# Performance work log

Measured on AMD Instinct MI355X. Metric: run time of the kernel, lower is better.

Reference implementation:

```python
import jax, jax.numpy as jnp
import numpy as np

B, T, D, A = 64, 2048, 512, 128

def setup_inputs() -> dict:
    key = jax.random.key(0)
    k_x, k_w1, k_b1, k_w2, k_b2 = jax.random.split(key, 5)
    s1 = 1.0 / np.sqrt(D)
    s2 = 1.0 / np.sqrt(A)
    return {
        "x": jax.random.normal(k_x, (B, T, D), dtype=jnp.float32),
        "W1": jax.random.uniform(k_w1, (D, A), minval=-s1, maxval=s1, dtype=jnp.float32),
        "b1": jax.random.uniform(k_b1, (A,), minval=-s1, maxval=s1, dtype=jnp.float32),
        "W2": jax.random.uniform(k_w2, (A, 1), minval=-s2, maxval=s2, dtype=jnp.float32),
        "b2": jax.random.uniform(k_b2, (1,), minval=-s2, maxval=s2, dtype=jnp.float32),
    }

def reference(x, W1, b1, W2, b2):
    # attention scores: [B, T, 1]
    h = jnp.tanh(jnp.einsum('btd,da->bta', x, W1) + b1)
    scores = jnp.einsum('bta,ao->bto', h, W2) + b2
    w = jax.nn.softmax(scores, axis=1)              # [B, T, 1]
    mu = jnp.sum(x * w, axis=1)                     # [B, D]
    var = jnp.sum((x - mu[:, None, :]) ** 2 * w, axis=1)
    std = jnp.sqrt(var + 1e-6)
    return jnp.concatenate([mu, std], axis=-1)      # [B, 2D]
```

## Files before the change

kernel.cpp:

```cpp
#include <hip/hip_runtime.h>
#include <hip/hip_bf16.h>
#include <math.h>

#define B_ 64
#define T_ 2048
#define D_ 512
#define A_ 128

typedef __bf16 bf16x8 __attribute__((ext_vector_type(8)));
typedef float  f32x4  __attribute__((ext_vector_type(4)));

__global__ __launch_bounds__(256) void prep_kernel(
    const float* __restrict__ W1, __hip_bfloat16* __restrict__ W1T)
{
    int idx = blockIdx.x * 256 + threadIdx.x;
    int k = idx >> 7;
    int n = idx & 127;
    W1T[n * D_ + k] = __float2bfloat16(W1[idx]);
}

__device__ inline bf16x8 cvt8(float4 a, float4 b) {
    bf16x8 r;
    r[0] = (__bf16)a.x; r[1] = (__bf16)a.y; r[2] = (__bf16)a.z; r[3] = (__bf16)a.w;
    r[4] = (__bf16)b.x; r[5] = (__bf16)b.y; r[6] = (__bf16)b.z; r[7] = (__bf16)b.w;
    return r;
}

__device__ inline float fast_tanh(float v) {
    v = fminf(fmaxf(v, -15.f), 15.f);
    float e = __expf(2.f * v);
    return (e - 1.f) / (e + 1.f);
}

__global__ __launch_bounds__(256) void scores_kernel(
    const float* __restrict__ x, const __hip_bfloat16* __restrict__ W1T_,
    const float* __restrict__ b1, const float* __restrict__ W2,
    const float* __restrict__ b2, float* __restrict__ scores)
{
    const __bf16* W1T = (const __bf16*)W1T_;
    const int tid  = threadIdx.x;
    const int wave = tid >> 6;
    const int lane = tid & 63;
    const int col  = lane & 15;
    const int kgrp = lane >> 4;

    const long tokbase = (long)blockIdx.x * 128 + wave * 32;

    f32x4 acc[8][2];
#pragma unroll
    for (int mt = 0; mt < 8; mt++) {
        acc[mt][0] = (f32x4){0.f, 0.f, 0.f, 0.f};
        acc[mt][1] = (f32x4){0.f, 0.f, 0.f, 0.f};
    }

    const float* xp0 = x + (tokbase + col) * D_;
    const float* xp1 = xp0 + 16 * D_;
    const __bf16* wp = W1T + (long)col * D_;

#pragma unroll 2
    for (int ks = 0; ks < 16; ks++) {
        const int klane = ks * 32 + kgrp * 8;
        float4 b0a = *(const float4*)(xp0 + klane);
        float4 b0b = *(const float4*)(xp0 + klane + 4);
        float4 b1a = *(const float4*)(xp1 + klane);
        float4 b1b = *(const float4*)(xp1 + klane + 4);
        bf16x8 bf0 = cvt8(b0a, b0b);
        bf16x8 bf1 = cvt8(b1a, b1b);
#pragma unroll
        for (int mt = 0; mt < 8; mt++) {
            bf16x8 af = *(const bf16x8*)(wp + (long)mt * 16 * D_ + klane);
            acc[mt][0] = __builtin_amdgcn_mfma_f32_16x16x32_bf16(af, bf0, acc[mt][0], 0, 0, 0);
            acc[mt][1] = __builtin_amdgcn_mfma_f32_16x16x32_bf16(af, bf1, acc[mt][1], 0, 0, 0);
        }
    }

    float p0 = 0.f, p1 = 0.f;
#pragma unroll
    for (int mt = 0; mt < 8; mt++) {
#pragma unroll
        for (int r = 0; r < 4; r++) {
            int n = mt * 16 + kgrp * 4 + r;
            float bb = b1[n];
            float ww = W2[n];
            p0 += fast_tanh(acc[mt][0][r] + bb) * ww;
            p1 += fast_tanh(acc[mt][1][r] + bb) * ww;
        }
    }
    p0 += __shfl_xor(p0, 16, 64);
    p0 += __shfl_xor(p0, 32, 64);
    p1 += __shfl_xor(p1, 16, 64);
    p1 += __shfl_xor(p1, 32, 64);
    if (lane < 16) {
        float bias = b2[0];
        scores[tokbase + col]      = p0 + bias;
        scores[tokbase + 16 + col] = p1 + bias;
    }
}

__global__ __launch_bounds__(256) void softmax_kernel(
    const float* __restrict__ scores, float* __restrict__ w)
{
    const int b = blockIdx.x;
    const int tid = threadIdx.x;
    const float* s = scores + (long)b * T_;

    float v[8];
    float mx = -1e30f;
#pragma unroll
    for (int j = 0; j < 8; j++) {
        v[j] = s[tid + j * 256];
        mx = fmaxf(mx, v[j]);
    }
#pragma unroll
    for (int off = 1; off < 64; off <<= 1)
        mx = fmaxf(mx, __shfl_xor(mx, off, 64));
    __shared__ float redm[4];
    if ((tid & 63) == 0) redm[tid >> 6] = mx;
    __syncthreads();
    mx = fmaxf(fmaxf(redm[0], redm[1]), fmaxf(redm[2], redm[3]));

    float sum = 0.f;
#pragma unroll
    for (int j = 0; j < 8; j++) {
        v[j] = __expf(v[j] - mx);
        sum += v[j];
    }
#pragma unroll
    for (int off = 1; off < 64; off <<= 1)
        sum += __shfl_xor(sum, off, 64);
    __shared__ float reds[4];
    if ((tid & 63) == 0) reds[tid >> 6] = sum;
    __syncthreads();
    sum = reds[0] + reds[1] + reds[2] + reds[3];
    const float inv = 1.0f / sum;
#pragma unroll
    for (int j = 0; j < 8; j++)
        w[(long)b * T_ + tid + j * 256] = v[j] * inv;
}

__global__ __launch_bounds__(256) void pool_partial_kernel(
    const float* __restrict__ x, const float* __restrict__ w,
    float* __restrict__ pmu, float* __restrict__ pm2)
{
    const int blk = blockIdx.x;
    const int b = blk >> 3;
    const int t0 = (blk & 7) * 256;
    const int tid = threadIdx.x;
    const int half = tid >> 7;
    const int dq = tid & 127;

    const float* wb = w + (long)b * T_ + t0;
    const float* xb = x + ((long)b * T_ + t0) * D_ + dq * 4;

    float4 mu = {0.f, 0.f, 0.f, 0.f};
    float4 m2 = {0.f, 0.f, 0.f, 0.f};

#pragma unroll 4
    for (int t = half; t < 256; t += 2) {
        float wt = wb[t];
        float4 xv = *(const float4*)(xb + (long)t * D_);
        mu.x = fmaf(wt, xv.x, mu.x);
        mu.y = fmaf(wt, xv.y, mu.y);
        mu.z = fmaf(wt, xv.z, mu.z);
        mu.w = fmaf(wt, xv.w, mu.w);
        m2.x = fmaf(wt * xv.x, xv.x, m2.x);
        m2.y = fmaf(wt * xv.y, xv.y, m2.y);
        m2.z = fmaf(wt * xv.z, xv.z, m2.z);
        m2.w = fmaf(wt * xv.w, xv.w, m2.w);
    }

    __shared__ float4 smu[256];
    __shared__ float4 sm2[256];
    smu[tid] = mu;
    sm2[tid] = m2;
    __syncthreads();

    if (tid < 128) {
        float4 a = smu[tid], c = smu[tid + 128];
        float4 e = sm2[tid], f = sm2[tid + 128];
        a.x += c.x; a.y += c.y; a.z += c.z; a.w += c.w;
        e.x += f.x; e.y += f.y; e.z += f.z; e.w += f.w;
        *(float4*)(pmu + (long)blk * D_ + dq * 4) = a;
        *(float4*)(pm2 + (long)blk * D_ + dq * 4) = e;
    }
}

__global__ __launch_bounds__(256) void pool_final_kernel(
    const float* __restrict__ pmu, const float* __restrict__ pm2,
    float* __restrict__ out)
{
    const int b = blockIdx.x;
    const int tid = threadIdx.x;
#pragma unroll
    for (int i = 0; i < 2; i++) {
        int d = tid + i * 256;
        float mu = 0.f, m2 = 0.f;
#pragma unroll
        for (int c = 0; c < 8; c++) {
            mu += pmu[((long)b * 8 + c) * D_ + d];
            m2 += pm2[((long)b * 8 + c) * D_ + d];
        }
        out[(long)b * (2 * D_) + d] = mu;
        out[(long)b * (2 * D_) + D_ + d] = sqrtf(fmaxf(m2 - mu * mu, 0.f) + 1e-6f);
    }
}

extern "C" void kernel_launch(void* const* d_in, const int* in_sizes, int n_in,
                              void* d_out, int out_size, void* d_ws, size_t ws_size,
                              hipStream_t stream) {
    const float* x  = (const float*)d_in[0];
    const float* W1 = (const float*)d_in[1];
    const float* b1 = (const float*)d_in[2];
    const float* W2 = (const float*)d_in[3];
    const float* b2 = (const float*)d_in[4];
    float* out = (float*)d_out;

    float* ws = (float*)d_ws;
    float* scores = ws;
    float* w      = ws + (long)B_ * T_;
    float* pmu    = ws + 2L * B_ * T_;
    float* pm2    = pmu + 512L * D_;
    __hip_bfloat16* W1T = (__hip_bfloat16*)(pm2 + 512L * D_);

    prep_kernel<<<256, 256, 0, stream>>>(W1, W1T);
    scores_kernel<<<(B_ * T_) / 128, 256, 0, stream>>>(x, W1T, b1, W2, b2, scores);
    softmax_kernel<<<B_, 256, 0, stream>>>(scores, w);
    pool_partial_kernel<<<B_ * 8, 256, 0, stream>>>(x, w, pmu, pm2);
    pool_final_kernel<<<B_, 256, 0, stream>>>(pmu, pm2, out);
}
```

Before: 428.2 us.

## Stage W1 in LDS and widen token tile per wave in scores kernel

The scores kernel now stages 128-column K chunks of the bf16 W1 transpose in padded shared memory and has each wave process 64 tokens instead of 32. Each W1 fragment then feeds four MFMAs instead of two, and the per-wave global reloads of W1 go away. The pooling partial kernel is split into 16 chunks per batch instead of 8 to raise parallelism, and the workspace offsets and final reduction are adjusted to match. The costs are more accumulator registers (a launch-bounds hint of 2 blocks per SM is added), extra barriers per K chunk, and half as many scores blocks.

```diff
diff --git a/kernel.cpp b/kernel.cpp
--- a/kernel.cpp
+++ b/kernel.cpp
@@ -18,6 +18,9 @@
     int n = idx & 127;
     W1T[n * D_ + k] = __float2bfloat16(W1[idx]);
 }
+
+#define KC 128
+#define KPAD 136
 
 __device__ inline bf16x8 cvt8(float4 a, float4 b) {
     bf16x8 r;
@@ -32,11 +35,13 @@
     return (e - 1.f) / (e + 1.f);
 }
 
-__global__ __launch_bounds__(256) void scores_kernel(
+__global__ __launch_bounds__(256, 2) void scores_kernel(
     const float* __restrict__ x, const __hip_bfloat16* __restrict__ W1T_,
     const float* __restrict__ b1, const float* __restrict__ W2,
     const float* __restrict__ b2, float* __restrict__ scores)
 {
+    __shared__ __bf16 w1s[A_][KPAD];
+
     const __bf16* W1T = (const __bf16*)W1T_;
     const int tid  = threadIdx.x;
     const int wave = tid >> 6;
@@ -44,37 +49,54 @@
     const int col  = lane & 15;
     const int kgrp = lane >> 4;
 
-    const long tokbase = (long)blockIdx.x * 128 + wave * 32;
-
-    f32x4 acc[8][2];
-#pragma unroll
-    for (int mt = 0; mt < 8; mt++) {
-        acc[mt][0] = (f32x4){0.f, 0.f, 0.f, 0.f};
-        acc[mt][1] = (f32x4){0.f, 0.f, 0.f, 0.f};
-    }
-
-    const float* xp0 = x + (tokbase + col) * D_;
-    const float* xp1 = xp0 + 16 * D_;
-    const __bf16* wp = W1T + (long)col * D_;
-
-#pragma unroll 2
-    for (int ks = 0; ks < 16; ks++) {
-        const int klane = ks * 32 + kgrp * 8;
-        float4 b0a = *(const float4*)(xp0 + klane);
-        float4 b0b = *(const float4*)(xp0 + klane + 4);
-        float4 b1a = *(const float4*)(xp1 + klane);
-        float4 b1b = *(const float4*)(xp1 + klane + 4);
-        bf16x8 bf0 = cvt8(b0a, b0b);
-        bf16x8 bf1 = cvt8(b1a, b1b);
-#pragma unroll
-        for (int mt = 0; mt < 8; mt++) {
-            bf16x8 af = *(const bf16x8*)(wp + (long)mt * 16 * D_ + klane);
-            acc[mt][0] = __builtin_amdgcn_mfma_f32_16x16x32_bf16(af, bf0, acc[mt][0], 0, 0, 0);
-            acc[mt][1] = __builtin_amdgcn_mfma_f32_16x16x32_bf16(af, bf1, acc[mt][1], 0, 0, 0);
-        }
-    }
-
-    float p0 = 0.f, p1 = 0.f;
+    const long tokbase = (long)blockIdx.x * 256 + wave * 64;
+
+    f32x4 acc[8][4];
+#pragma unroll
+    for (int mt = 0; mt < 8; mt++)
+#pragma unroll
+        for (int tt = 0; tt < 4; tt++)
+            acc[mt][tt] = (f32x4){0.f, 0.f, 0.f, 0.f};
+
+    const float* xp = x + (tokbase + col) * D_;
+
+    for (int kc = 0; kc < D_; kc += KC) {
+        __syncthreads();
+        {
+            int n = tid >> 4;
+#pragma unroll
+            for (int i = 0; i < 8; i++) {
+                int idx = tid + i * 256;
+                int row = idx >> 4;
+                int kslot = idx & 15;
+                *(bf16x8*)&w1s[row][kslot * 8] =
+                    *(const bf16x8*)(W1T + (long)row * D_ + kc + kslot * 8);
+            }
+            (void)n;
+        }
+        __syncthreads();
+
+#pragma unroll
+        for (int ks = 0; ks < 4; ks++) {
+            const int klane = kc + ks * 32 + kgrp * 8;
+            bf16x8 bf[4];
+#pragma unroll
+            for (int tt = 0; tt < 4; tt++) {
+                float4 a = *(const float4*)(xp + (long)tt * 16 * D_ + klane);
+                float4 b = *(const float4*)(xp + (long)tt * 16 * D_ + klane + 4);
+                bf[tt] = cvt8(a, b);
+            }
+#pragma unroll
+            for (int mt = 0; mt < 8; mt++) {
+                bf16x8 af = *(const bf16x8*)&w1s[mt * 16 + col][ks * 32 + kgrp * 8];
+#pragma unroll
+                for (int tt = 0; tt < 4; tt++)
+                    acc[mt][tt] = __builtin_amdgcn_mfma_f32_16x16x32_bf16(af, bf[tt], acc[mt][tt], 0, 0, 0);
+            }
+        }
+    }
+
+    float p[4] = {0.f, 0.f, 0.f, 0.f};
 #pragma unroll
     for (int mt = 0; mt < 8; mt++) {
 #pragma unroll
@@ -82,18 +104,21 @@
             int n = mt * 16 + kgrp * 4 + r;
             float bb = b1[n];
             float ww = W2[n];
-            p0 += fast_tanh(acc[mt][0][r] + bb) * ww;
-            p1 += fast_tanh(acc[mt][1][r] + bb) * ww;
-        }
-    }
-    p0 += __shfl_xor(p0, 16, 64);
-    p0 += __shfl_xor(p0, 32, 64);
-    p1 += __shfl_xor(p1, 16, 64);
-    p1 += __shfl_xor(p1, 32, 64);
+#pragma unroll
+            for (int tt = 0; tt < 4; tt++)
+                p[tt] += fast_tanh(acc[mt][tt][r] + bb) * ww;
+        }
+    }
+#pragma unroll
+    for (int tt = 0; tt < 4; tt++) {
+        p[tt] += __shfl_xor(p[tt], 16, 64);
+        p[tt] += __shfl_xor(p[tt], 32, 64);
+    }
     if (lane < 16) {
         float bias = b2[0];
-        scores[tokbase + col]      = p0 + bias;
-        scores[tokbase + 16 + col] = p1 + bias;
+#pragma unroll
+        for (int tt = 0; tt < 4; tt++)
+            scores[tokbase + tt * 16 + col] = p[tt] + bias;
     }
 }
 
@@ -143,8 +168,8 @@
     float* __restrict__ pmu, float* __restrict__ pm2)
 {
     const int blk = blockIdx.x;
-    const int b = blk >> 3;
-    const int t0 = (blk & 7) * 256;
+    const int b = blk >> 4;
+    const int t0 = (blk & 15) * 128;
     const int tid = threadIdx.x;
     const int half = tid >> 7;
     const int dq = tid & 127;
@@ -156,7 +181,7 @@
     float4 m2 = {0.f, 0.f, 0.f, 0.f};
 
 #pragma unroll 4
-    for (int t = half; t < 256; t += 2) {
+    for (int t = half; t < 128; t += 2) {
         float wt = wb[t];
         float4 xv = *(const float4*)(xb + (long)t * D_);
         mu.x = fmaf(wt, xv.x, mu.x);
@@ -196,9 +221,9 @@
         int d = tid + i * 256;
         float mu = 0.f, m2 = 0.f;
 #pragma unroll
-        for (int c = 0; c < 8; c++) {
-            mu += pmu[((long)b * 8 + c) * D_ + d];
-            m2 += pm2[((long)b * 8 + c) * D_ + d];
+        for (int c = 0; c < 16; c++) {
+            mu += pmu[((long)b * 16 + c) * D_ + d];
+            m2 += pm2[((long)b * 16 + c) * D_ + d];
         }
         out[(long)b * (2 * D_) + d] = mu;
         out[(long)b * (2 * D_) + D_ + d] = sqrtf(fmaxf(m2 - mu * mu, 0.f) + 1e-6f);
@@ -219,12 +244,12 @@
     float* scores = ws;
     float* w      = ws + (long)B_ * T_;
     float* pmu    = ws + 2L * B_ * T_;
-    float* pm2    = pmu + 512L * D_;
-    __hip_bfloat16* W1T = (__hip_bfloat16*)(pm2 + 512L * D_);
+    float* pm2    = pmu + 1024L * D_;
+    __hip_bfloat16* W1T = (__hip_bfloat16*)(pm2 + 1024L * D_);
 
     prep_kernel<<<256, 256, 0, stream>>>(W1, W1T);
-    scores_kernel<<<(B_ * T_) / 128, 256, 0, stream>>>(x, W1T, b1, W2, b2, scores);
+    scores_kernel<<<(B_ * T_) / 256, 256, 0, stream>>>(x, W1T, b1, W2, b2, scores);
     softmax_kernel<<<B_, 256, 0, stream>>>(scores, w);
-    pool_partial_kernel<<<B_ * 8, 256, 0, stream>>>(x, w, pmu, pm2);
+    pool_partial_kernel<<<B_ * 16, 256, 0, stream>>>(x, w, pmu, pm2);
     pool_final_kernel<<<B_, 256, 0, stream>>>(pmu, pm2, out);
 }
```

Result: slower. 445.1 us (+3.9%).

## Fuse scores, softmax and pooling into one chunked kernel with deferred normalization

Applied to the files above, without the earlier changes.

Merges the score GEMM, softmax and weighted pooling into one kernel per 64-token chunk. Each chunk computes unnormalized exp(score) weights and accumulates weighted partial sums, and the finalize kernel divides by the summed partition. The aim is to read x from HBM once instead of twice and to drop two kernel launches. The risk is that exp without max subtraction can overflow for large scores, and finalize now reduces 32 chunks per batch instead of 8.

```diff
diff --git a/kernel.cpp b/kernel.cpp
--- a/kernel.cpp
+++ b/kernel.cpp
@@ -6,6 +6,8 @@
 #define T_ 2048
 #define D_ 512
 #define A_ 128
+#define CHUNK 64
+#define NCHUNK (T_ / CHUNK)
 
 typedef __bf16 bf16x8 __attribute__((ext_vector_type(8)));
 typedef float  f32x4  __attribute__((ext_vector_type(4)));
@@ -32,10 +34,11 @@
     return (e - 1.f) / (e + 1.f);
 }
 
-__global__ __launch_bounds__(256) void scores_kernel(
+__global__ __launch_bounds__(256) void fused_kernel(
     const float* __restrict__ x, const __hip_bfloat16* __restrict__ W1T_,
     const float* __restrict__ b1, const float* __restrict__ W2,
-    const float* __restrict__ b2, float* __restrict__ scores)
+    const float* __restrict__ b2,
+    float* __restrict__ pmu, float* __restrict__ pm2, float* __restrict__ pz)
 {
     const __bf16* W1T = (const __bf16*)W1T_;
     const int tid  = threadIdx.x;
@@ -44,129 +47,64 @@
     const int col  = lane & 15;
     const int kgrp = lane >> 4;
 
-    const long tokbase = (long)blockIdx.x * 128 + wave * 32;
+    const int  blk = blockIdx.x;
+    const long tokbase = (long)blk * CHUNK + wave * 16;
 
-    f32x4 acc[8][2];
+    f32x4 acc[8];
 #pragma unroll
-    for (int mt = 0; mt < 8; mt++) {
-        acc[mt][0] = (f32x4){0.f, 0.f, 0.f, 0.f};
-        acc[mt][1] = (f32x4){0.f, 0.f, 0.f, 0.f};
-    }
+    for (int mt = 0; mt < 8; mt++) acc[mt] = (f32x4){0.f, 0.f, 0.f, 0.f};
 
-    const float* xp0 = x + (tokbase + col) * D_;
-    const float* xp1 = xp0 + 16 * D_;
+    const float* xp = x + (tokbase + col) * D_;
     const __bf16* wp = W1T + (long)col * D_;
 
-#pragma unroll 2
+#pragma unroll 4
     for (int ks = 0; ks < 16; ks++) {
         const int klane = ks * 32 + kgrp * 8;
-        float4 b0a = *(const float4*)(xp0 + klane);
-        float4 b0b = *(const float4*)(xp0 + klane + 4);
-        float4 b1a = *(const float4*)(xp1 + klane);
-        float4 b1b = *(const float4*)(xp1 + klane + 4);
-        bf16x8 bf0 = cvt8(b0a, b0b);
-        bf16x8 bf1 = cvt8(b1a, b1b);
+        float4 a0 = *(const float4*)(xp + klane);
+        float4 a1 = *(const float4*)(xp + klane + 4);
+        bf16x8 bf = cvt8(a0, a1);
 #pragma unroll
         for (int mt = 0; mt < 8; mt++) {
             bf16x8 af = *(const bf16x8*)(wp + (long)mt * 16 * D_ + klane);
-            acc[mt][0] = __builtin_amdgcn_mfma_f32_16x16x32_bf16(af, bf0, acc[mt][0], 0, 0, 0);
-            acc[mt][1] = __builtin_amdgcn_mfma_f32_16x16x32_bf16(af, bf1, acc[mt][1], 0, 0, 0);
+            acc[mt] = __builtin_amdgcn_mfma_f32_16x16x32_bf16(af, bf, acc[mt], 0, 0, 0);
         }
     }
 
-    float p0 = 0.f, p1 = 0.f;
+    float p = 0.f;
 #pragma unroll
     for (int mt = 0; mt < 8; mt++) {
 #pragma unroll
         for (int r = 0; r < 4; r++) {
             int n = mt * 16 + kgrp * 4 + r;
-            float bb = b1[n];
-            float ww = W2[n];
-            p0 += fast_tanh(acc[mt][0][r] + bb) * ww;
-            p1 += fast_tanh(acc[mt][1][r] + bb) * ww;
+            p += fast_tanh(acc[mt][r] + b1[n]) * W2[n];
         }
     }
-    p0 += __shfl_xor(p0, 16, 64);
-    p0 += __shfl_xor(p0, 32, 64);
-    p1 += __shfl_xor(p1, 16, 64);
-    p1 += __shfl_xor(p1, 32, 64);
-    if (lane < 16) {
-        float bias = b2[0];
-        scores[tokbase + col]      = p0 + bias;
-        scores[tokbase + 16 + col] = p1 + bias;
-    }
-}
+    p += __shfl_xor(p, 16, 64);
+    p += __shfl_xor(p, 32, 64);
 
-__global__ __launch_bounds__(256) void softmax_kernel(
-    const float* __restrict__ scores, float* __restrict__ w)
-{
-    const int b = blockIdx.x;
-    const int tid = threadIdx.x;
-    const float* s = scores + (long)b * T_;
+    __shared__ float se[CHUNK];
+    if (lane < 16)
+        se[wave * 16 + col] = __expf(p + b2[0]);
+    __syncthreads();
 
-    float v[8];
-    float mx = -1e30f;
-#pragma unroll
-    for (int j = 0; j < 8; j++) {
-        v[j] = s[tid + j * 256];
-        mx = fmaxf(mx, v[j]);
-    }
-#pragma unroll
-    for (int off = 1; off < 64; off <<= 1)
-        mx = fmaxf(mx, __shfl_xor(mx, off, 64));
-    __shared__ float redm[4];
-    if ((tid & 63) == 0) redm[tid >> 6] = mx;
-    __syncthreads();
-    mx = fmaxf(fmaxf(redm[0], redm[1]), fmaxf(redm[2], redm[3]));
-
-    float sum = 0.f;
-#pragma unroll
-    for (int j = 0; j < 8; j++) {
-        v[j] = __expf(v[j] - mx);
-        sum += v[j];
-    }
-#pragma unroll
-    for (int off = 1; off < 64; off <<= 1)
-        sum += __shfl_xor(sum, off, 64);
-    __shared__ float reds[4];
-    if ((tid & 63) == 0) reds[tid >> 6] = sum;
-    __syncthreads();
-    sum = reds[0] + reds[1] + reds[2] + reds[3];
-    const float inv = 1.0f / sum;
-#pragma unroll
-    for (int j = 0; j < 8; j++)
-        w[(long)b * T_ + tid + j * 256] = v[j] * inv;
-}
-
-__global__ __launch_bounds__(256) void pool_partial_kernel(
-    const float* __restrict__ x, const float* __restrict__ w,
-    float* __restrict__ pmu, float* __restrict__ pm2)
-{
-    const int blk = blockIdx.x;
-    const int b = blk >> 3;
-    const int t0 = (blk & 7) * 256;
-    const int tid = threadIdx.x;
-    const int half = tid >> 7;
+    const int tg = tid >> 7;
     const int dq = tid & 127;
-
-    const float* wb = w + (long)b * T_ + t0;
-    const float* xb = x + ((long)b * T_ + t0) * D_ + dq * 4;
+    const float* xb = x + (long)blk * CHUNK * D_ + dq * 4;
 
     float4 mu = {0.f, 0.f, 0.f, 0.f};
     float4 m2 = {0.f, 0.f, 0.f, 0.f};
-
 #pragma unroll 4
-    for (int t = half; t < 256; t += 2) {
-        float wt = wb[t];
+    for (int t = tg; t < CHUNK; t += 2) {
+        float e = se[t];
         float4 xv = *(const float4*)(xb + (long)t * D_);
-        mu.x = fmaf(wt, xv.x, mu.x);
-        mu.y = fmaf(wt, xv.y, mu.y);
-        mu.z = fmaf(wt, xv.z, mu.z);
-        mu.w = fmaf(wt, xv.w, mu.w);
-        m2.x = fmaf(wt * xv.x, xv.x, m2.x);
-        m2.y = fmaf(wt * xv.y, xv.y, m2.y);
-        m2.z = fmaf(wt * xv.z, xv.z, m2.z);
-        m2.w = fmaf(wt * xv.w, xv.w, m2.w);
+        mu.x = fmaf(e, xv.x, mu.x);
+        mu.y = fmaf(e, xv.y, mu.y);
+        mu.z = fmaf(e, xv.z, mu.z);
+        mu.w = fmaf(e, xv.w, mu.w);
+        m2.x = fmaf(e * xv.x, xv.x, m2.x);
+        m2.y = fmaf(e * xv.y, xv.y, m2.y);
+        m2.z = fmaf(e * xv.z, xv.z, m2.z);
+        m2.w = fmaf(e * xv.w, xv.w, m2.w);
     }
 
     __shared__ float4 smu[256];
@@ -183,23 +121,40 @@
         *(float4*)(pmu + (long)blk * D_ + dq * 4) = a;
         *(float4*)(pm2 + (long)blk * D_ + dq * 4) = e;
     }
+    if (tid == 0) {
+        float z = 0.f;
+#pragma unroll
+        for (int t = 0; t < CHUNK; t++) z += se[t];
+        pz[blk] = z;
+    }
 }
 
-__global__ __launch_bounds__(256) void pool_final_kernel(
+__global__ __launch_bounds__(256) void finalize_kernel(
     const float* __restrict__ pmu, const float* __restrict__ pm2,
-    float* __restrict__ out)
+    const float* __restrict__ pz, float* __restrict__ out)
 {
     const int b = blockIdx.x;
     const int tid = threadIdx.x;
+
+    __shared__ float zsh;
+    float z = (tid < NCHUNK) ? pz[b * NCHUNK + tid] : 0.f;
+#pragma unroll
+    for (int off = 1; off < 32; off <<= 1) z += __shfl_xor(z, off, 64);
+    if (tid == 0) zsh = z;
+    __syncthreads();
+    const float invz = 1.0f / zsh;
+
 #pragma unroll
     for (int i = 0; i < 2; i++) {
         int d = tid + i * 256;
         float mu = 0.f, m2 = 0.f;
 #pragma unroll
-        for (int c = 0; c < 8; c++) {
-            mu += pmu[((long)b * 8 + c) * D_ + d];
-            m2 += pm2[((long)b * 8 + c) * D_ + d];
+        for (int c = 0; c < NCHUNK; c++) {
+            mu += pmu[((long)b * NCHUNK + c) * D_ + d];
+            m2 += pm2[((long)b * NCHUNK + c) * D_ + d];
         }
+        mu *= invz;
+        m2 *= invz;
         out[(long)b * (2 * D_) + d] = mu;
         out[(long)b * (2 * D_) + D_ + d] = sqrtf(fmaxf(m2 - mu * mu, 0.f) + 1e-6f);
     }
@@ -215,16 +170,14 @@
     const float* b2 = (const float*)d_in[4];
     float* out = (float*)d_out;
 
+    const int nblk = (B_ * T_) / CHUNK;
     float* ws = (float*)d_ws;
-    float* scores = ws;
-    float* w      = ws + (long)B_ * T_;
-    float* pmu    = ws + 2L * B_ * T_;
-    float* pm2    = pmu + 512L * D_;
-    __hip_bfloat16* W1T = (__hip_bfloat16*)(pm2 + 512L * D_);
+    float* pmu = ws;
+    float* pm2 = pmu + (long)nblk * D_;
+    float* pz  = pm2 + (long)nblk * D_;
+    __hip_bfloat16* W1T = (__hip_bfloat16*)(pz + nblk);
 
     prep_kernel<<<256, 256, 0, stream>>>(W1, W1T);
-    scores_kernel<<<(B_ * T_) / 128, 256, 0, stream>>>(x, W1T, b1, W2, b2, scores);
-    softmax_kernel<<<B_, 256, 0, stream>>>(scores, w);
-    pool_partial_kernel<<<B_ * 8, 256, 0, stream>>>(x, w, pmu, pm2);
-    pool_final_kernel<<<B_, 256, 0, stream>>>(pmu, pm2, out);
+    fused_kernel<<<nblk, 256, 0, stream>>>(x, W1T, b1, W2, b2, pmu, pm2, pz);
+    finalize_kernel<<<B_, 256, 0, stream>>>(pmu, pm2, pz, out);
 }
```

Measured after the change: 473.9 us. 1.11x slower.
